# Kernel tuning notes

Hardware: AMD Instinct MI355X
Metric: run time of the kernel (lower is better)

## Reference

```python
import jax, jax.numpy as jnp
import numpy as np

NUM_CATEGORIES = 72
TEMPERATURE = 0.07
SEGMENT_WEIGHT = 10.0
MISSING_CATEGORIES = (13, 53, 61)
EPS = 1e-12
NEG_INF = -1e30


def setup_inputs() -> dict:
    key = jax.random.key(0)
    k1, k2 = jax.random.split(key)
    B, N, D = 4, 262144, 32
    embeddings = jax.random.normal(k1, (B, N, D), dtype=jnp.float32)
    segment_labels = jax.random.randint(k2, (B, N), 0, NUM_CATEGORIES, dtype=jnp.int64)
    return {"embeddings": embeddings, "segment_labels": segment_labels}


def _l2norm(x):
    return x / jnp.maximum(jnp.linalg.norm(x, axis=-1, keepdims=True), EPS)


def reference(embeddings, segment_labels):
    C = NUM_CATEGORIES
    missing = jnp.zeros((C,), dtype=bool).at[jnp.array(MISSING_CATEGORIES)].set(True)
    valid = segment_labels >= 0                      # [B,N]
    labels = jnp.clip(segment_labels, 0, C - 1)      # safe indices
    emb_n = _l2norm(embeddings)                      # [B,N,D]

    def per_batch(e, lab, v):
        w = v.astype(e.dtype)                                        # [N]
        counts = jax.ops.segment_sum(w, lab, num_segments=C)         # [C]
        sums = jax.ops.segment_sum(e * w[:, None], lab, num_segments=C)  # [C,D]
        protos = _l2norm(sums / jnp.maximum(counts, 1.0)[:, None])   # [C,D]
        present = (counts > 0) & (~missing)                          # [C]
        # similarity over all categories, mask absent/missing prototypes
        sim = jnp.einsum('nd,cd->nc', e, protos) / TEMPERATURE       # [N,C]
        logits = jnp.where(present[None, :], sim, NEG_INF)
        logp = jax.nn.log_softmax(logits, axis=-1)
        nll = -jnp.take_along_axis(logp, lab[:, None], axis=1)[:, 0]  # [N]
        keep = (v & (~missing[lab])).astype(e.dtype)                  # ignore_index=-100 analogue
        return jnp.sum(nll * keep) / jnp.maximum(jnp.sum(keep), 1.0)

    losses = jax.vmap(per_batch)(emb_n, labels, valid)  # [B]
    segment_loss = jnp.mean(losses)                     # segment_count == B here
    return SEGMENT_WEIGHT * segment_loss
```

## Files before the change

### kernel.cpp

```cpp
#include <hip/hip_runtime.h>
#include <hip/hip_bf16.h>

#define NCAT 72
#define NCATP 80
#define DIM 32
#define ROWS 36
#define BNUM 4
#define TEMP_INV (1.0f / 0.07f)
#define SEG_W 10.0f

#define WS_SUMS 0
#define WS_CNTS 9216
#define WS_PROT 9504
#define WS_NABS 19744
#define WS_LOSS 19748
#define WS_KEEP 19752
#define WS_TOTAL 19756

typedef __attribute__((ext_vector_type(8))) short short8v;
typedef __attribute__((ext_vector_type(4))) float f32x4;
typedef __attribute__((ext_vector_type(4))) unsigned u32x4;

__device__ __forceinline__ bool is_missing(int c) {
    return (c == 13) | (c == 53) | (c == 61);
}

__device__ __forceinline__ short f2bf_hi(float f, float* hi_f) {
    unsigned u = __float_as_uint(f);
    unsigned r = u + 0x7FFFu + ((u >> 16) & 1u);
    *hi_f = __uint_as_float(r & 0xFFFF0000u);
    return (short)(r >> 16);
}
__device__ __forceinline__ short f2bf(float f) {
    unsigned u = __float_as_uint(f);
    unsigned r = u + 0x7FFFu + ((u >> 16) & 1u);
    return (short)(r >> 16);
}

__device__ __forceinline__ unsigned cvtpk_bf16(float a, float b) {
    unsigned r;
    asm("v_cvt_pk_bf16_f32 %0, %1, %2" : "=v"(r) : "v"(a), "v"(b));
    return r;
}

template <int BPB>
__global__ __launch_bounds__(256) void k_accum(const float* __restrict__ emb,
                                               const int* __restrict__ lab,
                                               float* __restrict__ ws, int Nb) {
    __shared__ float s_acc[4][NCAT][ROWS];
    __shared__ float s_cnt[4][NCAT];
    __shared__ int   s_prb[4][NCAT];
    const int t = threadIdx.x;
    const int b = blockIdx.x / BPB;
    const int blk = blockIdx.x % BPB;
    const int w = t >> 6;
    const int g = (t >> 3) & 7;
    const int sub = t & 7;
    const int pofs = t >> 3;

    for (int i = t; i < 4 * NCAT * ROWS; i += 256) ((float*)s_acc)[i] = 0.f;
    for (int i = t; i < 4 * NCAT; i += 256) ((float*)s_cnt)[i] = 0.f;
    __syncthreads();

    float* accw = &s_acc[w][0][0];
    int* prbw = &s_prb[w][0];
    const float* eb = emb + (size_t)b * Nb * DIM;
    const int* lb = lab + (size_t)b * Nb;

    int p = blk * 32 + pofs;
    int l_cur = lb[p];
    float4 v_cur = ((const float4*)(eb + (size_t)p * DIM))[sub];

    for (int p0 = blk * 32; p0 < Nb; p0 += BPB * 32) {
        const int pn = p0 + BPB * 32 + pofs;
        int l_nxt = -1;
        float4 v_nxt = make_float4(0.f, 0.f, 0.f, 0.f);
        if (pn < Nb) {
            l_nxt = lb[pn];
            v_nxt = ((const float4*)(eb + (size_t)pn * DIM))[sub];
        }

        float ss = v_cur.x * v_cur.x + v_cur.y * v_cur.y +
                   v_cur.z * v_cur.z + v_cur.w * v_cur.w;
        ss += __shfl_xor(ss, 1);
        ss += __shfl_xor(ss, 2);
        ss += __shfl_xor(ss, 4);
        const float inv = 1.0f / fmaxf(sqrtf(ss), 1e-12f);
        const bool valid = (l_cur >= 0);
        const int lc = min(max(l_cur, 0), NCAT - 1);
        float4 u;
        u.x = v_cur.x * inv; u.y = v_cur.y * inv;
        u.z = v_cur.z * inv; u.w = v_cur.w * inv;

        if (valid && sub == 0) unsafeAtomicAdd(&s_cnt[w][lc], 1.0f);

        float* rowp = accw + lc * ROWS + sub * 4;
        bool active = valid;
        while (__any(active)) {
            asm volatile("" ::: "memory");
            if (active && sub == 0) prbw[lc] = g;
            int win = 0;
            if (active && sub == 0) win = (prbw[lc] == g) ? 1 : 0;
            const unsigned long long wb = __ballot(win);
            const bool iwin = active && ((wb >> (g * 8)) & 1ull);
            if (iwin) {
                float4* r4 = (float4*)rowp;
                float4 o = *r4;
                o.x += u.x; o.y += u.y; o.z += u.z; o.w += u.w;
                *r4 = o;
            }
            active = active && !iwin;
        }

        l_cur = l_nxt;
        v_cur = v_nxt;
    }
    __syncthreads();

    float* gs = ws + WS_SUMS + b * NCAT * DIM;
    for (int i = t; i < NCAT * DIM; i += 256) {
        const int c = i >> 5, d = i & 31;
        float val = s_acc[0][c][d] + s_acc[1][c][d] +
                    s_acc[2][c][d] + s_acc[3][c][d];
        if (val != 0.f) unsafeAtomicAdd(&gs[i], val);
    }
    if (t < NCAT) {
        float c = s_cnt[0][t] + s_cnt[1][t] + s_cnt[2][t] + s_cnt[3][t];
        if (c != 0.f) unsafeAtomicAdd(ws + WS_CNTS + b * NCAT + t, c);
    }
}

__global__ __launch_bounds__(256) void k_proto(float* __restrict__ ws) {
    const int b = blockIdx.x;
    __shared__ float s_np;
    if (threadIdx.x == 0) s_np = 0.f;
    __syncthreads();
    const float* gs = ws + WS_SUMS + b * NCAT * DIM;
    const float* gc = ws + WS_CNTS + b * NCAT;
    float* gp = ws + WS_PROT + b * NCATP * DIM;
    const int dd = threadIdx.x & 31;
    const int r0 = threadIdx.x >> 5;
    for (int c = r0; c < NCAT; c += 8) {
        float cnt = gc[c];
        float val = gs[c * DIM + dd] / fmaxf(cnt, 1.0f);
        float ss = val * val;
        #pragma unroll
        for (int m = 16; m >= 1; m >>= 1) ss += __shfl_xor(ss, m);
        float inv = 1.0f / fmaxf(sqrtf(ss), 1e-12f);
        const bool present = (cnt > 0.f) && !is_missing(c);
        gp[c * DIM + dd] = present ? val * inv : 0.f;
        if (dd == 0) unsafeAtomicAdd(&s_np, present ? 1.f : 0.f);
    }
    __syncthreads();
    if (threadIdx.x == 0) ws[WS_NABS + b] = (float)NCATP - s_np;
}

__device__ __forceinline__ void point_group(
    int pt, int l, const float* __restrict__ eb,
    const u32x4 (*__restrict__ sf)[64], int lane,
    float nabs, int sub, float& lacc, float& dacc, float& kacc)
{
    const float LOG2E = 1.4426950408889634f;
    const int lc = min(max(l, 0), NCAT - 1);

    const float4* ep = (const float4*)(eb + (size_t)pt * DIM + sub * 8);
    float4 a0 = ep[0], a1 = ep[1];

    float ea[8] = {a0.x, a0.y, a0.z, a0.w, a1.x, a1.y, a1.z, a1.w};
    u32x4 hw, lw;
    #pragma unroll
    for (int j = 0; j < 4; j++) {
        const float x0 = ea[2 * j], x1 = ea[2 * j + 1];
        const unsigned h = cvtpk_bf16(x0, x1);
        const float h0 = __uint_as_float(h << 16);
        const float h1 = __uint_as_float(h & 0xFFFF0000u);
        hw[j] = h;
        lw[j] = cvtpk_bf16(x0 - h0, x1 - h1);
    }
    const short8v ehi = __builtin_bit_cast(short8v, hw);
    const short8v elo = __builtin_bit_cast(short8v, lw);

    float ss = a0.x * a0.x + a0.y * a0.y + a0.z * a0.z + a0.w * a0.w +
               a1.x * a1.x + a1.y * a1.y + a1.z * a1.z + a1.w * a1.w;
    ss += __shfl_xor(ss, 16);
    ss += __shfl_xor(ss, 32);
    const float kk = (TEMP_INV * LOG2E) * __builtin_amdgcn_rsqf(fmaxf(ss, 1e-24f));

    const bool keep = (l >= 0) && !is_missing(lc);
    const int ltile = lc >> 4;
    const bool qm = keep && (((lc >> 2) & 3) == sub);

    float s = 0.f;
    #pragma unroll
    for (int n = 0; n < 5; n++) {
        const short8v phn = __builtin_bit_cast(short8v, sf[n * 2][lane]);
        const short8v pln = __builtin_bit_cast(short8v, sf[n * 2 + 1][lane]);
        f32x4 acc = {0.f, 0.f, 0.f, 0.f};
        acc = __builtin_amdgcn_mfma_f32_16x16x32_bf16(phn, ehi, acc, 0, 0, 0);
        acc = __builtin_amdgcn_mfma_f32_16x16x32_bf16(pln, ehi, acc, 0, 0, 0);
        acc = __builtin_amdgcn_mfma_f32_16x16x32_bf16(phn, elo, acc, 0, 0, 0);
        s += __builtin_amdgcn_exp2f(acc[0] * kk) + __builtin_amdgcn_exp2f(acc[1] * kk) +
             __builtin_amdgcn_exp2f(acc[2] * kk) + __builtin_amdgcn_exp2f(acc[3] * kk);
        if (qm && ltile == n) {
            const float d01 = (lc & 1) ? acc[1] : acc[0];
            const float d23 = (lc & 1) ? acc[3] : acc[2];
            dacc += kk * ((lc & 2) ? d23 : d01);
        }
    }
    s += __shfl_xor(s, 16);
    s += __shfl_xor(s, 32);
    s -= nabs;
    const float cl = __builtin_amdgcn_logf(s);
    if (keep && sub == 0) {
        lacc += cl;
        kacc += 1.f;
    }
}

template <int BPB>
__global__ __launch_bounds__(256, 4) void k_loss(const float* __restrict__ emb,
                                                 const int* __restrict__ lab,
                                                 const float* __restrict__ protos,
                                                 const float* __restrict__ nabsp,
                                                 float* __restrict__ lossout,
                                                 int Nb) {
    __shared__ u32x4 s_frag[10][64];
    __shared__ float s_red[8];
    const int b = blockIdx.x / BPB;
    const int blk = blockIdx.x % BPB;
    const int t = threadIdx.x;
    const int lane = t & 63;
    const int wave = t >> 6;
    const int lid = lane & 15;
    const int sub = lane >> 4;

    const float* pp = protos + b * NCATP * DIM;
    const float nabs = nabsp[b];
    const float* eb = emb + (size_t)b * Nb * DIM;
    const int* lb = lab + (size_t)b * Nb;
    const float LN2 = 0.6931471805599453f;

    if (wave == 0) {
        #pragma unroll
        for (int n = 0; n < 5; n++) {
            const int cat = n * 16 + lid;
            const float4* qk = (const float4*)(pp + cat * DIM + sub * 8);
            float4 q0 = qk[0], q1 = qk[1];
            float qa[8] = {q0.x, q0.y, q0.z, q0.w, q1.x, q1.y, q1.z, q1.w};
            short8v hi8, lo8;
            #pragma unroll
            for (int j = 0; j < 8; j++) {
                float hf;
                hi8[j] = f2bf_hi(qa[j], &hf);
                lo8[j] = f2bf(qa[j] - hf);
            }
            s_frag[n * 2][lane] = __builtin_bit_cast(u32x4, hi8);
            s_frag[n * 2 + 1][lane] = __builtin_bit_cast(u32x4, lo8);
        }
    }
    __syncthreads();

    float lacc = 0.f, dacc = 0.f, kacc = 0.f;

    #pragma unroll 1
    for (int p0 = (blk * 4 + wave) * 64; p0 < Nb; p0 += BPB * 4 * 64) {
        const int lv = lb[p0 + lane];
        const int l0 = __shfl(lv, lid);
        const int l1 = __shfl(lv, 16 + lid);
        const int l2 = __shfl(lv, 32 + lid);
        const int l3 = __shfl(lv, 48 + lid);
        point_group(p0 + lid,      l0, eb, s_frag, lane, nabs, sub, lacc, dacc, kacc);
        point_group(p0 + 16 + lid, l1, eb, s_frag, lane, nabs, sub, lacc, dacc, kacc);
        point_group(p0 + 32 + lid, l2, eb, s_frag, lane, nabs, sub, lacc, dacc, kacc);
        point_group(p0 + 48 + lid, l3, eb, s_frag, lane, nabs, sub, lacc, dacc, kacc);
    }

    float v = lacc - dacc;
    #pragma unroll
    for (int m = 32; m >= 1; m >>= 1) {
        v += __shfl_xor(v, m);
        kacc += __shfl_xor(kacc, m);
    }
    if (lane == 0) {
        s_red[wave] = v;
        s_red[4 + wave] = kacc;
    }
    __syncthreads();
    if (t == 0) {
        float a = s_red[0] + s_red[1] + s_red[2] + s_red[3];
        float k = s_red[4] + s_red[5] + s_red[6] + s_red[7];
        unsafeAtomicAdd(lossout + b, LN2 * a);
        unsafeAtomicAdd(lossout + BNUM + b, k);
    }
}

__global__ void k_final(const float* __restrict__ ws, float* __restrict__ out) {
    if (threadIdx.x == 0 && blockIdx.x == 0) {
        float s = 0.f;
        for (int b = 0; b < BNUM; b++) {
            float l = ws[WS_LOSS + b];
            float k = ws[WS_KEEP + b];
            s += l / fmaxf(k, 1.0f);
        }
        out[0] = SEG_W * (s / BNUM);
    }
}

extern "C" void kernel_launch(void* const* d_in, const int* in_sizes, int n_in,
                              void* d_out, int out_size, void* d_ws, size_t ws_size,
                              hipStream_t stream) {
    const float* emb = (const float*)d_in[0];
    const int* lab = (const int*)d_in[1];
    float* ws = (float*)d_ws;
    float* out = (float*)d_out;
    const int total_pts = in_sizes[1];
    const int Nb = total_pts / BNUM;

    hipMemsetAsync(d_ws, 0, WS_TOTAL * sizeof(float), stream);
    constexpr int BPB_ACC = 192;
    constexpr int BPB_LOSS = 256;
    k_accum<BPB_ACC><<<dim3(BNUM * BPB_ACC), dim3(256), 0, stream>>>(emb, lab, ws, Nb);
    k_proto<<<dim3(BNUM), dim3(256), 0, stream>>>(ws);
    k_loss<BPB_LOSS><<<dim3(BNUM * BPB_LOSS), dim3(256), 0, stream>>>(
        emb, lab, ws + WS_PROT, ws + WS_NABS, ws + WS_LOSS, Nb);
    k_final<<<1, 64, 0, stream>>>(ws, out);
}
```

Baseline: 113.0 us.

## Fuse prototype normalization into loss kernel and rank-based LDS conflict resolution

Removes the separate k_proto launch. Each k_loss block now normalizes the prototypes itself from the global sums and counts while building its bf16 fragments, and counts present categories with a ballot. The accumulate kernel drops the probe-and-retry loop for colliding LDS row updates. Each group instead computes its rank among groups sharing the same label via shuffles and writes in rank order. This saves one kernel launch and the spin loop's extra LDS traffic, at the cost of every loss block redoing the small prototype computation.

Result: faster. 110.2 us (-2.6%).

```diff
diff --git a/kernel.cpp b/kernel.cpp
--- a/kernel.cpp
+++ b/kernel.cpp
@@ -11,11 +11,9 @@
 
 #define WS_SUMS 0
 #define WS_CNTS 9216
-#define WS_PROT 9504
-#define WS_NABS 19744
-#define WS_LOSS 19748
-#define WS_KEEP 19752
-#define WS_TOTAL 19756
+#define WS_LOSS 9504
+#define WS_KEEP 9508
+#define WS_TOTAL 9512
 
 typedef __attribute__((ext_vector_type(8))) short short8v;
 typedef __attribute__((ext_vector_type(4))) float f32x4;
@@ -49,7 +47,6 @@
                                                float* __restrict__ ws, int Nb) {
     __shared__ float s_acc[4][NCAT][ROWS];
     __shared__ float s_cnt[4][NCAT];
-    __shared__ int   s_prb[4][NCAT];
     const int t = threadIdx.x;
     const int b = blockIdx.x / BPB;
     const int blk = blockIdx.x % BPB;
@@ -63,7 +60,6 @@
     __syncthreads();
 
     float* accw = &s_acc[w][0][0];
-    int* prbw = &s_prb[w][0];
     const float* eb = emb + (size_t)b * Nb * DIM;
     const int* lb = lab + (size_t)b * Nb;
 
@@ -80,14 +76,28 @@
             v_nxt = ((const float4*)(eb + (size_t)pn * DIM))[sub];
         }
 
+        const bool valid = (l_cur >= 0);
+        const int lc = min(max(l_cur, 0), NCAT - 1);
+        const int key = valid ? lc : (-1 - g);
+        const int k0 = __shfl(key, 0),  k1 = __shfl(key, 8);
+        const int k2 = __shfl(key, 16), k3 = __shfl(key, 24);
+        const int k4 = __shfl(key, 32), k5 = __shfl(key, 40);
+        const int k6 = __shfl(key, 48);
+        int myr = 0;
+        myr += (g > 0 && k0 == key);
+        myr += (g > 1 && k1 == key);
+        myr += (g > 2 && k2 == key);
+        myr += (g > 3 && k3 == key);
+        myr += (g > 4 && k4 == key);
+        myr += (g > 5 && k5 == key);
+        myr += (g > 6 && k6 == key);
+
         float ss = v_cur.x * v_cur.x + v_cur.y * v_cur.y +
                    v_cur.z * v_cur.z + v_cur.w * v_cur.w;
         ss += __shfl_xor(ss, 1);
         ss += __shfl_xor(ss, 2);
         ss += __shfl_xor(ss, 4);
         const float inv = 1.0f / fmaxf(sqrtf(ss), 1e-12f);
-        const bool valid = (l_cur >= 0);
-        const int lc = min(max(l_cur, 0), NCAT - 1);
         float4 u;
         u.x = v_cur.x * inv; u.y = v_cur.y * inv;
         u.z = v_cur.z * inv; u.w = v_cur.w * inv;
@@ -95,21 +105,15 @@
         if (valid && sub == 0) unsafeAtomicAdd(&s_cnt[w][lc], 1.0f);
 
         float* rowp = accw + lc * ROWS + sub * 4;
-        bool active = valid;
-        while (__any(active)) {
-            asm volatile("" ::: "memory");
-            if (active && sub == 0) prbw[lc] = g;
-            int win = 0;
-            if (active && sub == 0) win = (prbw[lc] == g) ? 1 : 0;
-            const unsigned long long wb = __ballot(win);
-            const bool iwin = active && ((wb >> (g * 8)) & 1ull);
-            if (iwin) {
+        for (int r = 0; ; ++r) {
+            if (valid && myr == r) {
                 float4* r4 = (float4*)rowp;
                 float4 o = *r4;
                 o.x += u.x; o.y += u.y; o.z += u.z; o.w += u.w;
                 *r4 = o;
             }
-            active = active && !iwin;
+            __builtin_amdgcn_sched_barrier(0);
+            if (!__any(valid && myr > r)) break;
         }
 
         l_cur = l_nxt;
@@ -128,31 +132,6 @@
         float c = s_cnt[0][t] + s_cnt[1][t] + s_cnt[2][t] + s_cnt[3][t];
         if (c != 0.f) unsafeAtomicAdd(ws + WS_CNTS + b * NCAT + t, c);
     }
-}
-
-__global__ __launch_bounds__(256) void k_proto(float* __restrict__ ws) {
-    const int b = blockIdx.x;
-    __shared__ float s_np;
-    if (threadIdx.x == 0) s_np = 0.f;
-    __syncthreads();
-    const float* gs = ws + WS_SUMS + b * NCAT * DIM;
-    const float* gc = ws + WS_CNTS + b * NCAT;
-    float* gp = ws + WS_PROT + b * NCATP * DIM;
-    const int dd = threadIdx.x & 31;
-    const int r0 = threadIdx.x >> 5;
-    for (int c = r0; c < NCAT; c += 8) {
-        float cnt = gc[c];
-        float val = gs[c * DIM + dd] / fmaxf(cnt, 1.0f);
-        float ss = val * val;
-        #pragma unroll
-        for (int m = 16; m >= 1; m >>= 1) ss += __shfl_xor(ss, m);
-        float inv = 1.0f / fmaxf(sqrtf(ss), 1e-12f);
-        const bool present = (cnt > 0.f) && !is_missing(c);
-        gp[c * DIM + dd] = present ? val * inv : 0.f;
-        if (dd == 0) unsafeAtomicAdd(&s_np, present ? 1.f : 0.f);
-    }
-    __syncthreads();
-    if (threadIdx.x == 0) ws[WS_NABS + b] = (float)NCATP - s_np;
 }
 
 __device__ __forceinline__ void point_group(
@@ -220,12 +199,12 @@
 template <int BPB>
 __global__ __launch_bounds__(256, 4) void k_loss(const float* __restrict__ emb,
                                                  const int* __restrict__ lab,
-                                                 const float* __restrict__ protos,
-                                                 const float* __restrict__ nabsp,
+                                                 const float* __restrict__ ws,
                                                  float* __restrict__ lossout,
                                                  int Nb) {
     __shared__ u32x4 s_frag[10][64];
     __shared__ float s_red[8];
+    __shared__ float s_nabs;
     const int b = blockIdx.x / BPB;
     const int blk = blockIdx.x % BPB;
     const int t = threadIdx.x;
@@ -234,31 +213,53 @@
     const int lid = lane & 15;
     const int sub = lane >> 4;
 
-    const float* pp = protos + b * NCATP * DIM;
-    const float nabs = nabsp[b];
     const float* eb = emb + (size_t)b * Nb * DIM;
     const int* lb = lab + (size_t)b * Nb;
     const float LN2 = 0.6931471805599453f;
 
     if (wave == 0) {
+        const float* gs = ws + WS_SUMS + b * NCAT * DIM;
+        const float* gc = ws + WS_CNTS + b * NCAT;
+        int np = 0;
         #pragma unroll
         for (int n = 0; n < 5; n++) {
             const int cat = n * 16 + lid;
-            const float4* qk = (const float4*)(pp + cat * DIM + sub * 8);
-            float4 q0 = qk[0], q1 = qk[1];
-            float qa[8] = {q0.x, q0.y, q0.z, q0.w, q1.x, q1.y, q1.z, q1.w};
+            float q[8];
+            float cnt = 0.f;
+            if (cat < NCAT) {
+                const float4* sp = (const float4*)(gs + cat * DIM + sub * 8);
+                float4 s0 = sp[0], s1 = sp[1];
+                cnt = gc[cat];
+                const float ic = 1.0f / fmaxf(cnt, 1.0f);
+                q[0] = s0.x * ic; q[1] = s0.y * ic; q[2] = s0.z * ic; q[3] = s0.w * ic;
+                q[4] = s1.x * ic; q[5] = s1.y * ic; q[6] = s1.z * ic; q[7] = s1.w * ic;
+            } else {
+                #pragma unroll
+                for (int j = 0; j < 8; j++) q[j] = 0.f;
+            }
+            float ss2 = 0.f;
+            #pragma unroll
+            for (int j = 0; j < 8; j++) ss2 += q[j] * q[j];
+            ss2 += __shfl_xor(ss2, 16);
+            ss2 += __shfl_xor(ss2, 32);
+            const bool present = (cat < NCAT) && (cnt > 0.f) && !is_missing(cat);
+            const float inv = present ? (1.0f / fmaxf(sqrtf(ss2), 1e-12f)) : 0.f;
             short8v hi8, lo8;
             #pragma unroll
             for (int j = 0; j < 8; j++) {
                 float hf;
-                hi8[j] = f2bf_hi(qa[j], &hf);
-                lo8[j] = f2bf(qa[j] - hf);
+                hi8[j] = f2bf_hi(q[j] * inv, &hf);
+                lo8[j] = f2bf(q[j] * inv - hf);
             }
             s_frag[n * 2][lane] = __builtin_bit_cast(u32x4, hi8);
             s_frag[n * 2 + 1][lane] = __builtin_bit_cast(u32x4, lo8);
-        }
+            const unsigned long long bal = __ballot(present && sub == 0);
+            np += (int)__popcll(bal & 0xFFFFull);
+        }
+        if (lane == 0) s_nabs = (float)(NCATP - np);
     }
     __syncthreads();
+    const float nabs = s_nabs;
 
     float lacc = 0.f, dacc = 0.f, kacc = 0.f;
 
@@ -320,8 +321,7 @@
     constexpr int BPB_ACC = 192;
     constexpr int BPB_LOSS = 256;
     k_accum<BPB_ACC><<<dim3(BNUM * BPB_ACC), dim3(256), 0, stream>>>(emb, lab, ws, Nb);
-    k_proto<<<dim3(BNUM), dim3(256), 0, stream>>>(ws);
     k_loss<BPB_LOSS><<<dim3(BNUM * BPB_LOSS), dim3(256), 0, stream>>>(
-        emb, lab, ws + WS_PROT, ws + WS_NABS, ws + WS_LOSS, Nb);
+        emb, lab, ws, ws + WS_LOSS, Nb);
     k_final<<<1, 64, 0, stream>>>(ws, out);
 }
```
